# Kernel tuning notes

Measured on AMD Instinct MI355X. Metric: run time of the kernel, lower is better.

Reference implementation:

```python
import jax, jax.numpy as jnp
import numpy as np
from jax import lax

EPS = 1e-5
SLOPE = 0.1
BETA = 0.25


def lrelu(x):
    return jnp.where(x >= 0, x, SLOPE * x)


def bn(x, g, b):
    # training-mode BatchNorm2d: batch stats over (N, H, W), biased variance
    m = x.mean((0, 2, 3), keepdims=True)
    v = x.var((0, 2, 3), keepdims=True)
    return g[None, :, None, None] * (x - m) * lax.rsqrt(v + EPS) + b[None, :, None, None]


def conv2d(x, w, b, stride=1, pad=1):
    y = lax.conv_general_dilated(x, w, (stride, stride), [(pad, pad), (pad, pad)],
                                 dimension_numbers=('NCHW', 'OIHW', 'NCHW'))
    return y + b[None, :, None, None]


def conv_transpose2d(x, w, b):
    # torch ConvTranspose2d(k=3, stride=2, padding=1, output_padding=1): out = 2*in
    # implemented as conv of stride-dilated input with spatially-flipped, IO-swapped kernel
    wt = jnp.flip(w, (2, 3)).transpose(1, 0, 2, 3)  # (in,out,kh,kw) -> (out,in,kh,kw)
    y = lax.conv_general_dilated(x, wt, (1, 1), [(1, 2), (1, 2)], lhs_dilation=(2, 2),
                                 dimension_numbers=('NCHW', 'OIHW', 'NCHW'))
    return y + b[None, :, None, None]


def vqvae_forward(x, cb, e1_w, e1_b, bn1_g, bn1_b, e2_w, e2_b, bn2_g, bn2_b,
                  preq_w, preq_b, postq_w, postq_b,
                  d1_w, d1_b, bn3_g, bn3_b, d2_w, d2_b, bn4_g, bn4_b, d3_w, d3_b):
    # encoder
    h = lrelu(bn(conv2d(x, e1_w, e1_b, stride=2), bn1_g, bn1_b))
    h = lrelu(bn(conv2d(h, e2_w, e2_b, stride=2), bn2_g, bn2_b))
    pq = conv2d(h, preq_w, preq_b)  # (B, cb_dim, H, W)
    B, C, H, W = pq.shape
    z = pq.transpose(0, 2, 3, 1).reshape(-1, C)  # (B*H*W, C)
    # squared euclidean distances (argmin equals cdist argmin)
    d2 = ((z * z).sum(-1, keepdims=True) - 2.0 * z @ cb.T + (cb * cb).sum(-1)[None, :])
    idx = jnp.argmin(d2, axis=-1)  # (B*H*W,)
    q = cb[idx]  # gather, (B*H*W, C)
    codebook_loss = jnp.mean((lax.stop_gradient(z) - q) ** 2)
    commitment_loss = jnp.mean((lax.stop_gradient(q) - z) ** 2)
    quantized_loss = codebook_loss + BETA * commitment_loss
    q_st = z + lax.stop_gradient(q - z)  # straight-through
    zq = q_st.reshape(B, H, W, C).transpose(0, 3, 1, 2)
    # decoder
    h = conv2d(zq, postq_w, postq_b)
    h = lrelu(bn(conv_transpose2d(h, d1_w, d1_b), bn3_g, bn3_b))
    h = lrelu(bn(conv_transpose2d(h, d2_w, d2_b), bn4_g, bn4_b))
    out = jnp.tanh(conv2d(h, d3_w, d3_b))
    return out, quantized_loss


def setup_inputs() -> dict:
    key = jax.random.key(0)
    ks = jax.random.split(key, 16)
    f32 = jnp.float32
    K, D, CC = 1024, 64, 3

    def w(k, shape, fan_in):
        return (jax.random.normal(k, shape, f32) / np.sqrt(fan_in)).astype(f32)

    inp = {
        'x': jax.random.normal(ks[0], (16, CC, 256, 256), f32),
        'cb': jax.random.normal(ks[1], (K, D), f32),
        'e1_w': w(ks[2], (16, CC, 3, 3), CC * 9), 'e1_b': jnp.zeros((16,), f32),
        'bn1_g': jnp.ones((16,), f32), 'bn1_b': jnp.zeros((16,), f32),
        'e2_w': w(ks[3], (4, 16, 3, 3), 16 * 9), 'e2_b': jnp.zeros((4,), f32),
        'bn2_g': jnp.ones((4,), f32), 'bn2_b': jnp.zeros((4,), f32),
        'preq_w': w(ks[4], (D, 4, 3, 3), 4 * 9), 'preq_b': jnp.zeros((D,), f32),
        'postq_w': w(ks[5], (4, D, 3, 3), D * 9), 'postq_b': jnp.zeros((4,), f32),
        'd1_w': w(ks[6], (4, 16, 3, 3), 4 * 9), 'd1_b': jnp.zeros((16,), f32),  # (in,out,kh,kw)
        'bn3_g': jnp.ones((16,), f32), 'bn3_b': jnp.zeros((16,), f32),
        'd2_w': w(ks[7], (16, 32, 3, 3), 16 * 9), 'd2_b': jnp.zeros((32,), f32),
        'bn4_g': jnp.ones((32,), f32), 'bn4_b': jnp.zeros((32,), f32),
        'd3_w': w(ks[8], (CC, 32, 3, 3), 32 * 9), 'd3_b': jnp.zeros((CC,), f32),
    }
    return inp


def reference(x, cb, e1_w, e1_b, bn1_g, bn1_b, e2_w, e2_b, bn2_g, bn2_b,
              preq_w, preq_b, postq_w, postq_b,
              d1_w, d1_b, bn3_g, bn3_b, d2_w, d2_b, bn4_g, bn4_b, d3_w, d3_b):
    return vqvae_forward(x, cb, e1_w, e1_b, bn1_g, bn1_b, e2_w, e2_b, bn2_g, bn2_b,
                         preq_w, preq_b, postq_w, postq_b,
                         d1_w, d1_b, bn3_g, bn3_b, d2_w, d2_b, bn4_g, bn4_b, d3_w, d3_b)
```

## Files before the change

kernel.cpp:

```cpp
#include <hip/hip_runtime.h>
#include <math.h>

#define EPSV 1e-5
#define SLOPE 0.1f

typedef __attribute__((ext_vector_type(4))) float f32x4;
typedef __attribute__((ext_vector_type(8))) short short8x;

__device__ __forceinline__ float lrelu(float x){ return x >= 0.f ? x : SLOPE * x; }
__device__ __forceinline__ float tanh_fast(float x){
  float e = __expf(2.f * x);
  return 1.f - 2.f / (e + 1.f);
}
__device__ __forceinline__ unsigned bf16rne(float f){
  unsigned u = __float_as_uint(f);
  u += 0x7fff + ((u >> 16) & 1);
  return u >> 16;
}

template<int CL>
__device__ __forceinline__ void stats_epilogue(const float* sums, const float* sqs,
    double* __restrict__ part, int chbase, int P, int p, float* sred){
  const int C2 = 2 * CL;
  int t = threadIdx.x;
  #pragma unroll
  for (int c = 0; c < CL; c++){
    sred[t * C2 + c] = sums[c];
    sred[t * C2 + CL + c] = sqs[c];
  }
  __syncthreads();
  if (t < 64){
    int c = t % C2;
    int g = t / C2;
    const int G = 64 / C2;
    const int R = 256 / G;
    double s = 0;
    for (int r = g * R; r < (g + 1) * R; r++) s += (double)sred[r * C2 + c];
    #pragma unroll
    for (int off = C2; off < 64; off <<= 1) s += __shfl_xor(s, off);
    if (t < C2){
      int ch = chbase + (c < CL ? c : c - CL);
      part[(size_t)ch * 2 * P + (c < CL ? 0 : P) + p] = s;
    }
  }
}

__global__ __launch_bounds__(256) void bn_red_fin(const double* __restrict__ part, int P,
    const float* __restrict__ g, const float* __restrict__ b, float* __restrict__ ss, int C, double count){
  int c = blockIdx.x;
  __shared__ double r0[256], r1[256];
  int t = threadIdx.x;
  double s = 0, q = 0;
  for (int p = t; p < P; p += 256){
    s += part[(size_t)c * 2 * P + p];
    q += part[(size_t)c * 2 * P + P + p];
  }
  r0[t] = s; r1[t] = q; __syncthreads();
  for (int o = 128; o > 0; o >>= 1){
    if (t < o){ r0[t] += r0[t + o]; r1[t] += r1[t + o]; }
    __syncthreads();
  }
  if (t == 0){
    double m = r0[0] / count;
    double var = r1[0] / count - m * m;
    double scale = (double)g[c] / sqrt(var + EPSV);
    ss[c] = (float)scale;
    ss[C + c] = (float)((double)b[c] - m * scale);
  }
}

__global__ __launch_bounds__(256) void e1_conv(const float* __restrict__ x, const float* __restrict__ w,
    const float* __restrict__ bias, float* __restrict__ out, double* __restrict__ part){
  int idx = blockIdx.x * 256 + threadIdx.x;
  int ox2 = idx & 63, oy = (idx >> 6) & 127, n = idx >> 13;
  float acc[16][2];
  #pragma unroll
  for (int co = 0; co < 16; co++){ float b = bias[co]; acc[co][0] = b; acc[co][1] = b; }
  int ix0 = 4 * ox2 - 1;
  int lclamp = (ox2 > 0) ? ix0 : 0;
  const float* xp = x + (size_t)n * 3 * 65536;
  #pragma unroll
  for (int ci = 0; ci < 3; ci++){
    const float* pl = xp + ci * 65536;
    #pragma unroll
    for (int ky = 0; ky < 3; ky++){
      int iy = 2 * oy - 1 + ky;
      if (iy >= 0){
        const float* row = pl + iy * 256;
        float l = row[lclamp];
        float4 m = *(const float4*)(row + ix0 + 1);
        float v0 = (ox2 > 0) ? l : 0.f;
        #pragma unroll
        for (int co = 0; co < 16; co++){
          const float* wp = w + ((co * 3 + ci) * 3 + ky) * 3;
          acc[co][0] = fmaf(v0,  wp[0], acc[co][0]);
          acc[co][0] = fmaf(m.x, wp[1], acc[co][0]);
          acc[co][0] = fmaf(m.y, wp[2], acc[co][0]);
          acc[co][1] = fmaf(m.y, wp[0], acc[co][1]);
          acc[co][1] = fmaf(m.z, wp[1], acc[co][1]);
          acc[co][1] = fmaf(m.w, wp[2], acc[co][1]);
        }
      }
    }
  }
  float sums[16], sqs[16];
  #pragma unroll
  for (int co = 0; co < 16; co++){
    float2 st; st.x = acc[co][0]; st.y = acc[co][1];
    *(float2*)(out + ((size_t)(n * 16 + co) * 128 + oy) * 128 + 2 * ox2) = st;
    sums[co] = acc[co][0] + acc[co][1];
    sqs[co] = acc[co][0] * acc[co][0] + acc[co][1] * acc[co][1];
  }
  __shared__ float sred[256 * 32];
  stats_epilogue<16>(sums, sqs, part, 0, 512, blockIdx.x, sred);
}

__global__ __launch_bounds__(256) void e2_conv(const float* __restrict__ in, const float* __restrict__ w,
    const float* __restrict__ bias, const float* __restrict__ ssIn, float* __restrict__ out,
    double* __restrict__ part){
  int idx = blockIdx.x * 256 + threadIdx.x;
  int ox = idx & 63, oy = (idx >> 6) & 63, n = idx >> 12;
  float acc[4];
  #pragma unroll
  for (int j = 0; j < 4; j++) acc[j] = bias[j];
  int iy0 = oy * 2 - 1, ix0 = ox * 2 - 1;
  const float* ip = in + (size_t)n * 16 * 16384;
  #pragma unroll
  for (int ky = 0; ky < 3; ky++){
    int iy = iy0 + ky; if ((unsigned)iy >= 128u) continue;
    #pragma unroll
    for (int kx = 0; kx < 3; kx++){
      int ix = ix0 + kx; if ((unsigned)ix >= 128u) continue;
      const float* r = ip + iy * 128 + ix;
      #pragma unroll
      for (int ci = 0; ci < 16; ci++){
        float v = lrelu(fmaf(r[ci * 16384], ssIn[ci], ssIn[16 + ci]));
        #pragma unroll
        for (int co = 0; co < 4; co++)
          acc[co] = fmaf(v, w[(co * 16 + ci) * 9 + ky * 3 + kx], acc[co]);
      }
    }
  }
  float sums[4], sqs[4];
  #pragma unroll
  for (int co = 0; co < 4; co++){
    out[(((size_t)n * 4 + co) * 64 + oy) * 64 + ox] = acc[co];
    sums[co] = acc[co];
    sqs[co] = acc[co] * acc[co];
  }
  __shared__ float sred[256 * 8];
  stats_epilogue<4>(sums, sqs, part, 0, 256, blockIdx.x, sred);
}

__global__ __launch_bounds__(256) void preq_conv(const float* __restrict__ in, const float* __restrict__ w,
    const float* __restrict__ bias, const float* __restrict__ ssIn, float* __restrict__ Zq){
  int idx = blockIdx.x * 256 + threadIdx.x;
  int sp = idx & 65535;
  int coq = idx >> 16;
  int x = sp & 63, y = (sp >> 6) & 63, n = sp >> 12;
  float scv[4] = {ssIn[0], ssIn[1], ssIn[2], ssIn[3]};
  float shv[4] = {ssIn[4], ssIn[5], ssIn[6], ssIn[7]};
  float a0 = bias[coq * 4 + 0], a1 = bias[coq * 4 + 1], a2 = bias[coq * 4 + 2], a3 = bias[coq * 4 + 3];
  const float* ip = in + (size_t)n * 4 * 4096;
  #pragma unroll
  for (int ky = 0; ky < 3; ky++){
    int iy = y - 1 + ky; if ((unsigned)iy >= 64u) continue;
    #pragma unroll
    for (int kx = 0; kx < 3; kx++){
      int ix = x - 1 + kx; if ((unsigned)ix >= 64u) continue;
      #pragma unroll
      for (int ci = 0; ci < 4; ci++){
        float v = lrelu(fmaf(ip[ci * 4096 + iy * 64 + ix], scv[ci], shv[ci]));
        const float* wp = w + ((coq * 4) * 4 + ci) * 9 + ky * 3 + kx;
        a0 = fmaf(v, wp[0], a0);
        a1 = fmaf(v, wp[36], a1);
        a2 = fmaf(v, wp[72], a2);
        a3 = fmaf(v, wp[108], a3);
      }
    }
  }
  float4 o; o.x = a0; o.y = a1; o.z = a2; o.w = a3;
  ((float4*)Zq)[coq * 65536 + sp] = o;
}

__global__ __launch_bounds__(256) void prep_all(const float* __restrict__ cb, double* __restrict__ cb64,
    double* __restrict__ cbn64, float* __restrict__ cbn32, unsigned short* __restrict__ cbh,
    unsigned short* __restrict__ cbl, int* __restrict__ flagcnt,
    const float* __restrict__ pw, float* __restrict__ P){
  int t = threadIdx.x;
  if (blockIdx.x < 4){
    int k = blockIdx.x * 256 + t;
    if (k == 0) flagcnt[0] = 0;
    double s = 0;
    for (int d = 0; d < 64; d++){
      float v = cb[k * 64 + d];
      cb64[(size_t)k * 64 + d] = (double)v;
      s = fma((double)v, (double)v, s);
      unsigned h = bf16rne(v);
      float hf = __uint_as_float(h << 16);
      unsigned l = bf16rne(v - hf);
      cbh[k * 64 + d] = (unsigned short)h;
      cbl[k * 64 + d] = (unsigned short)l;
    }
    cbn64[k] = s;
    cbn32[k] = (float)s;
  } else {
    int gid = (blockIdx.x - 4) * 256 + t;
    if (gid >= 9216) return;
    int k = gid / 9, tap = gid - k * 9;
    float a0 = 0.f, a1 = 0.f, a2 = 0.f, a3 = 0.f;
    const float* cp = cb + (k << 6);
    #pragma unroll 16
    for (int ci = 0; ci < 64; ci++){
      float c = cp[ci];
      a0 = fmaf(c, pw[(0 * 64 + ci) * 9 + tap], a0);
      a1 = fmaf(c, pw[(1 * 64 + ci) * 9 + tap], a1);
      a2 = fmaf(c, pw[(2 * 64 + ci) * 9 + tap], a2);
      a3 = fmaf(c, pw[(3 * 64 + ci) * 9 + tap], a3);
    }
    float4 o; o.x = a0; o.y = a1; o.z = a2; o.w = a3;
    ((float4*)P)[gid] = o;
  }
}

__global__ __launch_bounds__(256) void vq_screen_mfma(const float* __restrict__ Zq,
    const unsigned short* __restrict__ cbh, const unsigned short* __restrict__ cbl,
    const float* __restrict__ cbn32, int* __restrict__ idxout,
    int* __restrict__ flagcnt, int* __restrict__ flaglist){
  __shared__ unsigned short lcb[32 * 64 * 8];
  __shared__ float lcn[128];
  int t = threadIdx.x;
  int lane = t & 63;
  int w = t >> 6;
  int col = lane & 15, hg = lane >> 4;
  int pos0 = blockIdx.x * 128 + w * 32;
  int posA = pos0 + col, posB = pos0 + 16 + col;
  const float4* Zq4 = (const float4*)Zq;
  short8x zhA[2], zlA[2], zhB[2], zlB[2];
  #pragma unroll
  for (int kc = 0; kc < 2; kc++){
    #pragma unroll
    for (int s = 0; s < 2; s++){
      int pos = s ? posB : posA;
      float4 f0 = Zq4[(size_t)(8 * kc + 2 * hg) * 65536 + pos];
      float4 f1 = Zq4[(size_t)(8 * kc + 2 * hg + 1) * 65536 + pos];
      float zv[8] = {f0.x, f0.y, f0.z, f0.w, f1.x, f1.y, f1.z, f1.w};
      union { unsigned u[4]; short8x v; } H, L;
      #pragma unroll
      for (int j = 0; j < 4; j++){
        unsigned h0 = bf16rne(zv[2 * j]);
        unsigned h1 = bf16rne(zv[2 * j + 1]);
        float hf0 = __uint_as_float(h0 << 16);
        float hf1 = __uint_as_float(h1 << 16);
        unsigned l0 = bf16rne(zv[2 * j] - hf0);
        unsigned l1 = bf16rne(zv[2 * j + 1] - hf1);
        H.u[j] = h0 | (h1 << 16);
        L.u[j] = l0 | (l1 << 16);
      }
      if (s){ zhB[kc] = H.v; zlB[kc] = L.v; } else { zhA[kc] = H.v; zlA[kc] = L.v; }
    }
  }
  float bestA = 3.0e38f, secA = 3.0e38f, bestB = 3.0e38f, secB = 3.0e38f;
  int biA = 0, biB = 0;
  for (int step = 0; step < 8; step++){
    int code0 = step * 128;
    __syncthreads();
    #pragma unroll
    for (int i = 0; i < 8; i++){
      int piece = i * 256 + t;
      int fb = piece >> 6, pl = piece & 63;
      int g = fb >> 2, kc = (fb >> 1) & 1, sp = fb & 1;
      const unsigned short* src = (sp ? cbl : cbh)
          + ((size_t)(code0 + g * 16 + (pl & 15)) << 6) + kc * 32 + ((pl >> 4) << 3);
      *(uint4*)&lcb[piece * 8] = *(const uint4*)src;
    }
    if (t < 128) lcn[t] = cbn32[code0 + t];
    __syncthreads();
    #pragma unroll 2
    for (int g = 0; g < 8; g++){
      const short8x* lc8 = (const short8x*)lcb;
      short8x Ah0 = lc8[(g * 4 + 0) * 64 + lane];
      short8x Al0 = lc8[(g * 4 + 1) * 64 + lane];
      short8x Ah1 = lc8[(g * 4 + 2) * 64 + lane];
      short8x Al1 = lc8[(g * 4 + 3) * 64 + lane];
      f32x4 accA = {0.f, 0.f, 0.f, 0.f};
      f32x4 accB = {0.f, 0.f, 0.f, 0.f};
      accA = __builtin_amdgcn_mfma_f32_16x16x32_bf16(Ah0, zhA[0], accA, 0, 0, 0);
      accA = __builtin_amdgcn_mfma_f32_16x16x32_bf16(Ah1, zhA[1], accA, 0, 0, 0);
      accA = __builtin_amdgcn_mfma_f32_16x16x32_bf16(Ah0, zlA[0], accA, 0, 0, 0);
      accA = __builtin_amdgcn_mfma_f32_16x16x32_bf16(Ah1, zlA[1], accA, 0, 0, 0);
      accA = __builtin_amdgcn_mfma_f32_16x16x32_bf16(Al0, zhA[0], accA, 0, 0, 0);
      accA = __builtin_amdgcn_mfma_f32_16x16x32_bf16(Al1, zhA[1], accA, 0, 0, 0);
      accB = __builtin_amdgcn_mfma_f32_16x16x32_bf16(Ah0, zhB[0], accB, 0, 0, 0);
      accB = __builtin_amdgcn_mfma_f32_16x16x32_bf16(Ah1, zhB[1], accB, 0, 0, 0);
      accB = __builtin_amdgcn_mfma_f32_16x16x32_bf16(Ah0, zlB[0], accB, 0, 0, 0);
      accB = __builtin_amdgcn_mfma_f32_16x16x32_bf16(Ah1, zlB[1], accB, 0, 0, 0);
      accB = __builtin_amdgcn_mfma_f32_16x16x32_bf16(Al0, zhB[0], accB, 0, 0, 0);
      accB = __builtin_amdgcn_mfma_f32_16x16x32_bf16(Al1, zhB[1], accB, 0, 0, 0);
      int cbase = code0 + g * 16 + 4 * hg;
      #pragma unroll
      for (int r = 0; r < 4; r++){
        float cn = lcn[g * 16 + 4 * hg + r];
        float sA = fmaf(accA[r], -2.0f, cn);
        float mA = fmaxf(sA, bestA);
        secA = fminf(secA, mA);
        if (sA < bestA){ bestA = sA; biA = cbase + r; }
        float sB = fmaf(accB[r], -2.0f, cn);
        float mB = fmaxf(sB, bestB);
        secB = fminf(secB, mB);
        if (sB < bestB){ bestB = sB; biB = cbase + r; }
      }
    }
  }
  #pragma unroll
  for (int off = 16; off <= 32; off <<= 1){
    float ob = __shfl_xor(bestA, off);
    float os = __shfl_xor(secA, off);
    int oi = __shfl_xor(biA, off);
    secA = fminf(fminf(secA, os), fmaxf(bestA, ob));
    if (ob < bestA){ bestA = ob; biA = oi; }
    ob = __shfl_xor(bestB, off);
    os = __shfl_xor(secB, off);
    oi = __shfl_xor(biB, off);
    secB = fminf(fminf(secB, os), fmaxf(bestB, ob));
    if (ob < bestB){ bestB = ob; biB = oi; }
  }
  if (hg == 0){
    idxout[posA] = biA;
    if (secA - bestA < 1.2e-2f){
      int slot = atomicAdd(flagcnt, 1);
      flaglist[slot] = posA;
    }
    idxout[posB] = biB;
    if (secB - bestB < 1.2e-2f){
      int slot = atomicAdd(flagcnt, 1);
      flaglist[slot] = posB;
    }
  }
}

__global__ __launch_bounds__(256) void vq_refine(const float* __restrict__ Zq, const double* __restrict__ cb64,
    const double* __restrict__ cbn64, const int* __restrict__ flagcnt, const int* __restrict__ flaglist,
    int* __restrict__ idxout){
  int gw = (blockIdx.x * 256 + threadIdx.x) >> 6;
  int lane = threadIdx.x & 63;
  int nf = flagcnt[0];
  for (int f = gw; f < nf; f += 512){
    int pos = flaglist[f];
    float zr[64];
    #pragma unroll
    for (int q = 0; q < 16; q++){
      float4 v = ((const float4*)Zq)[q * 65536 + pos];
      zr[4 * q] = v.x; zr[4 * q + 1] = v.y; zr[4 * q + 2] = v.z; zr[4 * q + 3] = v.w;
    }
    double best = 1e300; int bi = 1 << 30;
    for (int k = lane; k < 1024; k += 64){
      const double* c = cb64 + (size_t)k * 64;
      double a0 = 0, a1 = 0, a2 = 0, a3 = 0;
      #pragma unroll
      for (int d = 0; d < 64; d += 4){
        a0 = fma(c[d], (double)zr[d], a0);
        a1 = fma(c[d + 1], (double)zr[d + 1], a1);
        a2 = fma(c[d + 2], (double)zr[d + 2], a2);
        a3 = fma(c[d + 3], (double)zr[d + 3], a3);
      }
      double s = cbn64[k] - 2.0 * ((a0 + a1) + (a2 + a3));
      if (s < best){ best = s; bi = k; }
    }
    #pragma unroll
    for (int o = 32; o > 0; o >>= 1){
      double ob = __shfl_xor(best, o);
      int oi = __shfl_xor(bi, o);
      if (ob < best || (ob == best && oi < bi)){ best = ob; bi = oi; }
    }
    if (lane == 0) idxout[pos] = bi;
  }
}

__global__ __launch_bounds__(256) void postq_gather(const float* __restrict__ P, const int* __restrict__ idxm,
    const float* __restrict__ bias, float* __restrict__ out,
    const float* __restrict__ Zq, const float* __restrict__ cb, double* __restrict__ losspart){
  int gid = blockIdx.x * 256 + threadIdx.x;
  int sp = gid & 65535;
  int co = gid >> 16;
  co = __builtin_amdgcn_readfirstlane(co);
  int xx = sp & 63, yy = (sp >> 6) & 63, n = sp >> 12;
  float acc = bias[co];
  #pragma unroll
  for (int ky = 0; ky < 3; ky++){
    int iy = yy - 1 + ky; if ((unsigned)iy >= 64u) continue;
    #pragma unroll
    for (int kx = 0; kx < 3; kx++){
      int ix = xx - 1 + kx; if ((unsigned)ix >= 64u) continue;
      int spt = (n << 12) + (iy << 6) + ix;
      int k = idxm[spt];
      acc += P[(k * 9 + (ky * 3 + kx)) * 4 + co];
    }
  }
  out[((size_t)(n * 4 + co) << 12) + (yy << 6) + xx] = acc;
  if (co == 0){
    int k = idxm[sp];
    const float4* c4 = (const float4*)(cb + (k << 6));
    double l = 0;
    #pragma unroll
    for (int q = 0; q < 16; q++){
      float4 z = ((const float4*)Zq)[q * 65536 + sp];
      float4 c = c4[q];
      float d0 = z.x - c.x, d1 = z.y - c.y, d2 = z.z - c.z, d3 = z.w - c.w;
      l += (double)d0 * d0 + (double)d1 * d1 + (double)d2 * d2 + (double)d3 * d3;
    }
    __shared__ double sb[256];
    int t = threadIdx.x;
    sb[t] = l; __syncthreads();
    for (int o = 128; o > 0; o >>= 1){
      if (t < o) sb[t] += sb[t + o];
      __syncthreads();
    }
    if (t == 0) losspart[blockIdx.x] = sb[0];
  }
}

template<int CI, int CO, int IHt, int IWt, bool APPLY>
__global__ __launch_bounds__(256) void convT_cob8(const float* __restrict__ in, const float* __restrict__ w,
    const float* __restrict__ bias, const float* __restrict__ ssIn, float* __restrict__ out,
    double* __restrict__ part){
  constexpr int SB = IHt * IWt / 256;
  constexpr int COG = CO / 8;
  constexpr int P = 16 * SB;
  const int OW = IWt * 2;
  int idx = blockIdx.x * 256 + threadIdx.x;
  int ix = idx % IWt, iy = (idx / IWt) % IHt;
  int cog = (idx / (IWt * IHt)) % COG, n = idx / (IWt * IHt * COG);
  cog = __builtin_amdgcn_readfirstlane(cog);
  n   = __builtin_amdgcn_readfirstlane(n);
  float a00[8], a01[8], a10[8], a11[8];
  #pragma unroll
  for (int j = 0; j < 8; j++){ float b = bias[cog * 8 + j]; a00[j] = b; a01[j] = b; a10[j] = b; a11[j] = b; }
  bool okx = (ix + 1 < IWt), oky = (iy + 1 < IHt);
  int ixp = okx ? ix + 1 : ix, iyp = oky ? iy + 1 : iy;
  const float* ip = in + (size_t)n * CI * IHt * IWt;
  #pragma unroll 4
  for (int ci = 0; ci < CI; ci++){
    const float* p = ip + ci * IHt * IWt;
    float v00 = p[iy * IWt + ix];
    float v01 = p[iy * IWt + ixp];
    float v10 = p[iyp * IWt + ix];
    float v11 = p[iyp * IWt + ixp];
    if (APPLY){
      float sc = ssIn[ci], sh = ssIn[CI + ci];
      v00 = lrelu(fmaf(v00, sc, sh));
      v01 = lrelu(fmaf(v01, sc, sh));
      v10 = lrelu(fmaf(v10, sc, sh));
      v11 = lrelu(fmaf(v11, sc, sh));
    }
    if (!okx) v01 = 0.f;
    if (!oky) v10 = 0.f;
    if (!(okx && oky)) v11 = 0.f;
    const float* wp = w + ((size_t)ci * CO + cog * 8) * 9;
    #pragma unroll
    for (int j = 0; j < 8; j++){
      const float* q = wp + j * 9;
      a00[j] = fmaf(q[4], v00, a00[j]);
      a01[j] = fmaf(q[3], v01, a01[j]); a01[j] = fmaf(q[5], v00, a01[j]);
      a10[j] = fmaf(q[1], v10, a10[j]); a10[j] = fmaf(q[7], v00, a10[j]);
      a11[j] = fmaf(q[0], v11, a11[j]); a11[j] = fmaf(q[2], v10, a11[j]);
      a11[j] = fmaf(q[6], v01, a11[j]); a11[j] = fmaf(q[8], v00, a11[j]);
    }
  }
  float sums[8], sqs[8];
  #pragma unroll
  for (int j = 0; j < 8; j++){
    float* o = out + (((size_t)n * CO + cog * 8 + j) * (IHt * 2) + 2 * iy) * OW + 2 * ix;
    float2 r0; r0.x = a00[j]; r0.y = a01[j];
    float2 r1; r1.x = a10[j]; r1.y = a11[j];
    *(float2*)o = r0;
    *(float2*)(o + OW) = r1;
    sums[j] = (a00[j] + a01[j]) + (a10[j] + a11[j]);
    sqs[j] = (a00[j] * a00[j] + a01[j] * a01[j]) + (a10[j] * a10[j] + a11[j] * a11[j]);
  }
  __shared__ float sred[256 * 16];
  int sb = blockIdx.x % SB;
  stats_epilogue<8>(sums, sqs, part, cog * 8, P, n * SB + sb, sred);
}

__global__ __launch_bounds__(256) void d3_tile(const float* __restrict__ F, const float* __restrict__ w,
    const float* __restrict__ bias, const float* __restrict__ ss, float* __restrict__ out,
    const double* __restrict__ losspart){
  __shared__ float st[4 * 6 * 256];
  int t = threadIdx.x;
  int xg = t & 63, r = t >> 6;
  int n = blockIdx.x >> 6, oyb = blockIdx.x & 63;
  int oy = oyb * 4 + r;
  if (blockIdx.x == 0 && t < 64){
    double s = losspart[t] + losspart[t + 64] + losspart[t + 128] + losspart[t + 192];
    #pragma unroll
    for (int o = 32; o > 0; o >>= 1) s += __shfl_xor(s, o);
    if (t == 0) out[3145728] = (float)(1.25 * s / (65536.0 * 64.0));
  }
  float acc[3][4];
  #pragma unroll
  for (int co = 0; co < 3; co++){
    float b = bias[co];
    #pragma unroll
    for (int j = 0; j < 4; j++) acc[co][j] = b;
  }
  const float* base = F + (size_t)n * 32 * 65536;
  for (int cc = 0; cc < 8; cc++){
    int cib = cc * 4;
    #pragma unroll
    for (int j = 0; j < 6; j++){
      int p = j * 256 + t;
      int cl = p / 384, rem = p - cl * 384;
      int rr = rem >> 6, xq = rem & 63;
      int g = oyb * 4 - 1 + rr;
      float4 v;
      if ((unsigned)g < 256u){
        v = *(const float4*)(base + ((size_t)(cib + cl) * 256 + g) * 256 + 4 * xq);
        float sc = ss[cib + cl], sh = ss[32 + cib + cl];
        v.x = lrelu(fmaf(v.x, sc, sh));
        v.y = lrelu(fmaf(v.y, sc, sh));
        v.z = lrelu(fmaf(v.z, sc, sh));
        v.w = lrelu(fmaf(v.w, sc, sh));
      } else {
        v.x = 0.f; v.y = 0.f; v.z = 0.f; v.w = 0.f;
      }
      *(float4*)&st[((cl * 6 + rr) << 8) | (4 * xq)] = v;
    }
    __syncthreads();
    #pragma unroll
    for (int cl = 0; cl < 4; cl++){
      #pragma unroll
      for (int ky = 0; ky < 3; ky++){
        int rr = r + ky;
        float4 A = *(const float4*)&st[((cl * 6 + rr) << 8) | (4 * xg)];
        float Lv = __shfl_up(A.w, 1);
        float Rv = __shfl_down(A.x, 1);
        float u0 = (xg == 0) ? 0.f : Lv;
        float u5 = (xg == 63) ? 0.f : Rv;
        float u[6] = {u0, A.x, A.y, A.z, A.w, u5};
        #pragma unroll
        for (int co = 0; co < 3; co++){
          const float* wp = w + ((co * 32 + cib + cl) * 9) + ky * 3;
          #pragma unroll
          for (int j = 0; j < 4; j++){
            acc[co][j] = fmaf(u[j],     wp[0], acc[co][j]);
            acc[co][j] = fmaf(u[j + 1], wp[1], acc[co][j]);
            acc[co][j] = fmaf(u[j + 2], wp[2], acc[co][j]);
          }
        }
      }
    }
    __syncthreads();
  }
  #pragma unroll
  for (int co = 0; co < 3; co++){
    float4 s0;
    s0.x = tanh_fast(acc[co][0]); s0.y = tanh_fast(acc[co][1]);
    s0.z = tanh_fast(acc[co][2]); s0.w = tanh_fast(acc[co][3]);
    float* o = out + ((size_t)(n * 3 + co) * 256 + oy) * 256 + 4 * xg;
    *(float4*)o = s0;
  }
}

extern "C" void kernel_launch(void* const* d_in, const int* in_sizes, int n_in,
                              void* d_out, int out_size, void* d_ws, size_t ws_size,
                              hipStream_t stream){
  const float* x      = (const float*)d_in[0];
  const float* cb     = (const float*)d_in[1];
  const float* e1_w   = (const float*)d_in[2];
  const float* e1_b   = (const float*)d_in[3];
  const float* bn1_g  = (const float*)d_in[4];
  const float* bn1_b  = (const float*)d_in[5];
  const float* e2_w   = (const float*)d_in[6];
  const float* e2_b   = (const float*)d_in[7];
  const float* bn2_g  = (const float*)d_in[8];
  const float* bn2_b  = (const float*)d_in[9];
  const float* preq_w = (const float*)d_in[10];
  const float* preq_b = (const float*)d_in[11];
  const float* postq_w= (const float*)d_in[12];
  const float* postq_b= (const float*)d_in[13];
  const float* d1_w   = (const float*)d_in[14];
  const float* d1_b   = (const float*)d_in[15];
  const float* bn3_g  = (const float*)d_in[16];
  const float* bn3_b  = (const float*)d_in[17];
  const float* d2_w   = (const float*)d_in[18];
  const float* d2_b   = (const float*)d_in[19];
  const float* bn4_g  = (const float*)d_in[20];
  const float* bn4_b  = (const float*)d_in[21];
  const float* d3_w   = (const float*)d_in[22];
  const float* d3_b   = (const float*)d_in[23];
  float* out = (float*)d_out;
  char* ws = (char*)d_ws;

  double* losspart = (double*)ws;
  int*    flagcnt  = (int*)(ws + 2048);
  float*  ss       = (float*)(ws + 4096);
  double* cb64     = (double*)(ws + 8192);
  double* cbn64    = (double*)(ws + 532480);
  float*  cbn32    = (float*)(ws + 540672);
  unsigned short* cbh = (unsigned short*)(ws + 544768);
  unsigned short* cbl = (unsigned short*)(ws + 675840);
  int*    flaglist = (int*)(ws + 806912);
  int*    idx      = (int*)(ws + 1069056);
  double* part_e1  = (double*)(ws + 1331200);
  double* part_e2  = (double*)(ws + 1462272);
  float*  Ptab     = (float*)(ws + 1478656);
  double* part_d1  = (double*)(ws + 1478656);
  double* part_d2  = (double*)(ws + 1544192);
  float*  A        = (float*)(ws + 2097152);
  float*  B        = (float*)(ws + 18874368);
  float*  Zq       = (float*)(ws + 19922944);
  float*  F        = (float*)(ws + 36700160);

  float *ss1 = ss + 0, *ss2 = ss + 32, *ss3 = ss + 48, *ss4 = ss + 80;
  float* D = B;

  prep_all<<<40, 256, 0, stream>>>(cb, cb64, cbn64, cbn32, cbh, cbl, flagcnt, postq_w, Ptab);

  e1_conv<<<512, 256, 0, stream>>>(x, e1_w, e1_b, A, part_e1);
  bn_red_fin<<<16, 256, 0, stream>>>(part_e1, 512, bn1_g, bn1_b, ss1, 16, 262144.0);
  e2_conv<<<256, 256, 0, stream>>>(A, e2_w, e2_b, ss1, B, part_e2);
  bn_red_fin<<<4, 256, 0, stream>>>(part_e2, 256, bn2_g, bn2_b, ss2, 4, 65536.0);
  preq_conv<<<4096, 256, 0, stream>>>(B, preq_w, preq_b, ss2, Zq);

  vq_screen_mfma<<<512, 256, 0, stream>>>(Zq, cbh, cbl, cbn32, idx, flagcnt, flaglist);
  vq_refine<<<128, 256, 0, stream>>>(Zq, cb64, cbn64, flagcnt, flaglist, idx);

  postq_gather<<<1024, 256, 0, stream>>>(Ptab, idx, postq_b, D, Zq, cb, losspart);
  convT_cob8<4, 16, 64, 64, false><<<512, 256, 0, stream>>>(D, d1_w, d1_b, nullptr, A, part_d1);
  bn_red_fin<<<16, 256, 0, stream>>>(part_d1, 256, bn3_g, bn3_b, ss3, 16, 262144.0);
  convT_cob8<16, 32, 128, 128, true><<<4096, 256, 0, stream>>>(A, d2_w, d2_b, ss3, F, part_d2);
  bn_red_fin<<<32, 256, 0, stream>>>(part_d2, 1024, bn4_g, bn4_b, ss4, 32, 1048576.0);
  d3_tile<<<1024, 256, 0, stream>>>(F, d3_w, d3_b, ss4, out, losspart);
}
```

Measured before the change: 308.0 us.

## Prune VQ refine to candidate code chunks and widen convT to two input columns

The screen kernel now writes each position's per-128-code-chunk best distance to a workspace buffer. The refine kernel reads these values and runs fp64 distances only for chunks whose best lies within the ambiguity margin, instead of scanning all 1024 codes. Separately, the transposed-conv kernel now has each thread handle two adjacent input columns, sharing loads and emitting float4 stores, with half the blocks. This adds register pressure and extra workspace traffic, and relies on the chunk-level bound being a safe pruning test.

```diff
diff --git a/kernel.cpp b/kernel.cpp
--- a/kernel.cpp
+++ b/kernel.cpp
@@ -226,7 +226,7 @@
 __global__ __launch_bounds__(256) void vq_screen_mfma(const float* __restrict__ Zq,
     const unsigned short* __restrict__ cbh, const unsigned short* __restrict__ cbl,
     const float* __restrict__ cbn32, int* __restrict__ idxout,
-    int* __restrict__ flagcnt, int* __restrict__ flaglist){
+    int* __restrict__ flagcnt, int* __restrict__ flaglist, float* __restrict__ stepb){
   __shared__ unsigned short lcb[32 * 64 * 8];
   __shared__ float lcn[128];
   int t = threadIdx.x;
@@ -240,8 +240,8 @@
   #pragma unroll
   for (int kc = 0; kc < 2; kc++){
     #pragma unroll
-    for (int s = 0; s < 2; s++){
-      int pos = s ? posB : posA;
+    for (int tb = 0; tb < 2; tb++){
+      int pos = tb ? posB : posA;
       float4 f0 = Zq4[(size_t)(8 * kc + 2 * hg) * 65536 + pos];
       float4 f1 = Zq4[(size_t)(8 * kc + 2 * hg + 1) * 65536 + pos];
       float zv[8] = {f0.x, f0.y, f0.z, f0.w, f1.x, f1.y, f1.z, f1.w};
@@ -257,11 +257,11 @@
         H.u[j] = h0 | (h1 << 16);
         L.u[j] = l0 | (l1 << 16);
       }
-      if (s){ zhB[kc] = H.v; zlB[kc] = L.v; } else { zhA[kc] = H.v; zlA[kc] = L.v; }
-    }
-  }
-  float bestA = 3.0e38f, secA = 3.0e38f, bestB = 3.0e38f, secB = 3.0e38f;
-  int biA = 0, biB = 0;
+      if (tb){ zhB[kc] = H.v; zlB[kc] = L.v; } else { zhA[kc] = H.v; zlA[kc] = L.v; }
+    }
+  }
+  float BA = 3.0e38f, SA = 3.0e38f, BB = 3.0e38f, SBt = 3.0e38f;
+  int IA = 0, IB = 0;
   for (int step = 0; step < 8; step++){
     int code0 = step * 128;
     __syncthreads();
@@ -276,6 +276,8 @@
     }
     if (t < 128) lcn[t] = cbn32[code0 + t];
     __syncthreads();
+    float bA = 3.0e38f, sA = 3.0e38f, bB = 3.0e38f, sB = 3.0e38f;
+    int iA = 0, iB = 0;
     #pragma unroll 2
     for (int g = 0; g < 8; g++){
       const short8x* lc8 = (const short8x*)lcb;
@@ -301,38 +303,42 @@
       #pragma unroll
       for (int r = 0; r < 4; r++){
         float cn = lcn[g * 16 + 4 * hg + r];
-        float sA = fmaf(accA[r], -2.0f, cn);
-        float mA = fmaxf(sA, bestA);
-        secA = fminf(secA, mA);
-        if (sA < bestA){ bestA = sA; biA = cbase + r; }
-        float sB = fmaf(accB[r], -2.0f, cn);
-        float mB = fmaxf(sB, bestB);
-        secB = fminf(secB, mB);
-        if (sB < bestB){ bestB = sB; biB = cbase + r; }
-      }
-    }
-  }
-  #pragma unroll
-  for (int off = 16; off <= 32; off <<= 1){
-    float ob = __shfl_xor(bestA, off);
-    float os = __shfl_xor(secA, off);
-    int oi = __shfl_xor(biA, off);
-    secA = fminf(fminf(secA, os), fmaxf(bestA, ob));
-    if (ob < bestA){ bestA = ob; biA = oi; }
-    ob = __shfl_xor(bestB, off);
-    os = __shfl_xor(secB, off);
-    oi = __shfl_xor(biB, off);
-    secB = fminf(fminf(secB, os), fmaxf(bestB, ob));
-    if (ob < bestB){ bestB = ob; biB = oi; }
+        float vA = fmaf(accA[r], -2.0f, cn);
+        sA = fminf(sA, fmaxf(vA, bA));
+        if (vA < bA){ bA = vA; iA = cbase + r; }
+        float vB = fmaf(accB[r], -2.0f, cn);
+        sB = fminf(sB, fmaxf(vB, bB));
+        if (vB < bB){ bB = vB; iB = cbase + r; }
+      }
+    }
+    #pragma unroll
+    for (int off = 16; off <= 32; off <<= 1){
+      float ob = __shfl_xor(bA, off);
+      float os = __shfl_xor(sA, off);
+      int oi = __shfl_xor(iA, off);
+      sA = fminf(fminf(sA, os), fmaxf(bA, ob));
+      if (ob < bA){ bA = ob; iA = oi; }
+      ob = __shfl_xor(bB, off);
+      os = __shfl_xor(sB, off);
+      oi = __shfl_xor(iB, off);
+      sB = fminf(fminf(sB, os), fmaxf(bB, ob));
+      if (ob < bB){ bB = ob; iB = oi; }
+    }
+    if (hg == 0){
+      stepb[step * 65536 + posA] = bA;
+      stepb[step * 65536 + posB] = bB;
+    }
+    if (bA < BA){ SA = fminf(BA, sA); BA = bA; IA = iA; } else SA = fminf(SA, bA);
+    if (bB < BB){ SBt = fminf(BB, sB); BB = bB; IB = iB; } else SBt = fminf(SBt, bB);
   }
   if (hg == 0){
-    idxout[posA] = biA;
-    if (secA - bestA < 1.2e-2f){
+    idxout[posA] = IA;
+    if (SA - BA < 1.2e-2f){
       int slot = atomicAdd(flagcnt, 1);
       flaglist[slot] = posA;
     }
-    idxout[posB] = biB;
-    if (secB - bestB < 1.2e-2f){
+    idxout[posB] = IB;
+    if (SBt - BB < 1.2e-2f){
       int slot = atomicAdd(flagcnt, 1);
       flaglist[slot] = posB;
     }
@@ -341,7 +347,7 @@
 
 __global__ __launch_bounds__(256) void vq_refine(const float* __restrict__ Zq, const double* __restrict__ cb64,
     const double* __restrict__ cbn64, const int* __restrict__ flagcnt, const int* __restrict__ flaglist,
-    int* __restrict__ idxout){
+    const float* __restrict__ stepb, int* __restrict__ idxout){
   int gw = (blockIdx.x * 256 + threadIdx.x) >> 6;
   int lane = threadIdx.x & 63;
   int nf = flagcnt[0];
@@ -353,19 +359,32 @@
       float4 v = ((const float4*)Zq)[q * 65536 + pos];
       zr[4 * q] = v.x; zr[4 * q + 1] = v.y; zr[4 * q + 2] = v.z; zr[4 * q + 3] = v.w;
     }
+    float sb[8];
+    float B = 3.0e38f;
+    #pragma unroll
+    for (int s = 0; s < 8; s++){ sb[s] = stepb[s * 65536 + pos]; B = fminf(B, sb[s]); }
+    float lim = B + 1.2e-2f;
     double best = 1e300; int bi = 1 << 30;
-    for (int k = lane; k < 1024; k += 64){
-      const double* c = cb64 + (size_t)k * 64;
-      double a0 = 0, a1 = 0, a2 = 0, a3 = 0;
-      #pragma unroll
-      for (int d = 0; d < 64; d += 4){
-        a0 = fma(c[d], (double)zr[d], a0);
-        a1 = fma(c[d + 1], (double)zr[d + 1], a1);
-        a2 = fma(c[d + 2], (double)zr[d + 2], a2);
-        a3 = fma(c[d + 3], (double)zr[d + 3], a3);
-      }
-      double s = cbn64[k] - 2.0 * ((a0 + a1) + (a2 + a3));
-      if (s < best){ best = s; bi = k; }
+    #pragma unroll
+    for (int s = 0; s < 8; s++){
+      if (sb[s] < lim){
+        int k0 = s * 128 + 2 * lane;
+        #pragma unroll
+        for (int kk = 0; kk < 2; kk++){
+          int k = k0 + kk;
+          const double* c = cb64 + (size_t)k * 64;
+          double a0 = 0, a1 = 0, a2 = 0, a3 = 0;
+          #pragma unroll
+          for (int d = 0; d < 64; d += 4){
+            a0 = fma(c[d], (double)zr[d], a0);
+            a1 = fma(c[d + 1], (double)zr[d + 1], a1);
+            a2 = fma(c[d + 2], (double)zr[d + 2], a2);
+            a3 = fma(c[d + 3], (double)zr[d + 3], a3);
+          }
+          double sc = cbn64[k] - 2.0 * ((a0 + a1) + (a2 + a3));
+          if (sc < best){ best = sc; bi = k; }
+        }
+      }
     }
     #pragma unroll
     for (int o = 32; o > 0; o >>= 1){
@@ -421,66 +440,82 @@
 }
 
 template<int CI, int CO, int IHt, int IWt, bool APPLY>
-__global__ __launch_bounds__(256) void convT_cob8(const float* __restrict__ in, const float* __restrict__ w,
+__global__ __launch_bounds__(256) void convT_w2(const float* __restrict__ in, const float* __restrict__ w,
     const float* __restrict__ bias, const float* __restrict__ ssIn, float* __restrict__ out,
     double* __restrict__ part){
-  constexpr int SB = IHt * IWt / 256;
+  constexpr int IWH = IWt / 2;
   constexpr int COG = CO / 8;
+  constexpr int SB = IHt * IWH * COG / 256;
   constexpr int P = 16 * SB;
   const int OW = IWt * 2;
   int idx = blockIdx.x * 256 + threadIdx.x;
-  int ix = idx % IWt, iy = (idx / IWt) % IHt;
-  int cog = (idx / (IWt * IHt)) % COG, n = idx / (IWt * IHt * COG);
+  int ixp = idx % IWH;
+  int iy = (idx / IWH) % IHt;
+  int cog = (idx / (IWH * IHt)) % COG;
+  int n = idx / (IWH * IHt * COG);
   cog = __builtin_amdgcn_readfirstlane(cog);
   n   = __builtin_amdgcn_readfirstlane(n);
-  float a00[8], a01[8], a10[8], a11[8];
-  #pragma unroll
-  for (int j = 0; j < 8; j++){ float b = bias[cog * 8 + j]; a00[j] = b; a01[j] = b; a10[j] = b; a11[j] = b; }
-  bool okx = (ix + 1 < IWt), oky = (iy + 1 < IHt);
-  int ixp = okx ? ix + 1 : ix, iyp = oky ? iy + 1 : iy;
+  float a[8][8];
+  #pragma unroll
+  for (int j = 0; j < 8; j++){
+    float b = bias[cog * 8 + j];
+    #pragma unroll
+    for (int q = 0; q < 8; q++) a[j][q] = b;
+  }
+  bool oky = (iy + 1 < IHt);
+  bool okx = (2 * ixp + 2 < IWt);
+  int iyp = oky ? iy + 1 : iy;
+  int xe = okx ? 2 : 0;
   const float* ip = in + (size_t)n * CI * IHt * IWt;
   #pragma unroll 4
   for (int ci = 0; ci < CI; ci++){
-    const float* p = ip + ci * IHt * IWt;
-    float v00 = p[iy * IWt + ix];
-    float v01 = p[iy * IWt + ixp];
-    float v10 = p[iyp * IWt + ix];
-    float v11 = p[iyp * IWt + ixp];
+    const float* r0 = ip + ci * IHt * IWt + iy * IWt + 2 * ixp;
+    const float* r1 = ip + ci * IHt * IWt + iyp * IWt + 2 * ixp;
+    float2 va = *(const float2*)r0;
+    float ve = r0[xe];
+    float2 vb = *(const float2*)r1;
+    float vf = r1[xe];
     if (APPLY){
       float sc = ssIn[ci], sh = ssIn[CI + ci];
-      v00 = lrelu(fmaf(v00, sc, sh));
-      v01 = lrelu(fmaf(v01, sc, sh));
-      v10 = lrelu(fmaf(v10, sc, sh));
-      v11 = lrelu(fmaf(v11, sc, sh));
-    }
-    if (!okx) v01 = 0.f;
-    if (!oky) v10 = 0.f;
-    if (!(okx && oky)) v11 = 0.f;
+      va.x = lrelu(fmaf(va.x, sc, sh));
+      va.y = lrelu(fmaf(va.y, sc, sh));
+      ve   = lrelu(fmaf(ve,   sc, sh));
+      vb.x = lrelu(fmaf(vb.x, sc, sh));
+      vb.y = lrelu(fmaf(vb.y, sc, sh));
+      vf   = lrelu(fmaf(vf,   sc, sh));
+    }
+    if (!okx){ ve = 0.f; vf = 0.f; }
+    if (!oky){ vb.x = 0.f; vb.y = 0.f; vf = 0.f; }
     const float* wp = w + ((size_t)ci * CO + cog * 8) * 9;
     #pragma unroll
     for (int j = 0; j < 8; j++){
       const float* q = wp + j * 9;
-      a00[j] = fmaf(q[4], v00, a00[j]);
-      a01[j] = fmaf(q[3], v01, a01[j]); a01[j] = fmaf(q[5], v00, a01[j]);
-      a10[j] = fmaf(q[1], v10, a10[j]); a10[j] = fmaf(q[7], v00, a10[j]);
-      a11[j] = fmaf(q[0], v11, a11[j]); a11[j] = fmaf(q[2], v10, a11[j]);
-      a11[j] = fmaf(q[6], v01, a11[j]); a11[j] = fmaf(q[8], v00, a11[j]);
+      a[j][0] = fmaf(q[4], va.x, a[j][0]);
+      a[j][1] = fmaf(q[3], va.y, a[j][1]); a[j][1] = fmaf(q[5], va.x, a[j][1]);
+      a[j][2] = fmaf(q[1], vb.x, a[j][2]); a[j][2] = fmaf(q[7], va.x, a[j][2]);
+      a[j][3] = fmaf(q[0], vb.y, a[j][3]); a[j][3] = fmaf(q[2], vb.x, a[j][3]);
+      a[j][3] = fmaf(q[6], va.y, a[j][3]); a[j][3] = fmaf(q[8], va.x, a[j][3]);
+      a[j][4] = fmaf(q[4], va.y, a[j][4]);
+      a[j][5] = fmaf(q[3], ve,   a[j][5]); a[j][5] = fmaf(q[5], va.y, a[j][5]);
+      a[j][6] = fmaf(q[1], vb.y, a[j][6]); a[j][6] = fmaf(q[7], va.y, a[j][6]);
+      a[j][7] = fmaf(q[0], vf,   a[j][7]); a[j][7] = fmaf(q[2], vb.y, a[j][7]);
+      a[j][7] = fmaf(q[6], ve,   a[j][7]); a[j][7] = fmaf(q[8], va.y, a[j][7]);
     }
   }
   float sums[8], sqs[8];
   #pragma unroll
   for (int j = 0; j < 8; j++){
-    float* o = out + (((size_t)n * CO + cog * 8 + j) * (IHt * 2) + 2 * iy) * OW + 2 * ix;
-    float2 r0; r0.x = a00[j]; r0.y = a01[j];
-    float2 r1; r1.x = a10[j]; r1.y = a11[j];
-    *(float2*)o = r0;
-    *(float2*)(o + OW) = r1;
-    sums[j] = (a00[j] + a01[j]) + (a10[j] + a11[j]);
-    sqs[j] = (a00[j] * a00[j] + a01[j] * a01[j]) + (a10[j] * a10[j] + a11[j] * a11[j]);
+    float4 R0; R0.x = a[j][0]; R0.y = a[j][1]; R0.z = a[j][4]; R0.w = a[j][5];
+    float4 R1; R1.x = a[j][2]; R1.y = a[j][3]; R1.z = a[j][6]; R1.w = a[j][7];
+    float* o = out + (((size_t)n * CO + cog * 8 + j) * (IHt * 2) + 2 * iy) * OW + 4 * ixp;
+    *(float4*)o = R0;
+    *(float4*)(o + OW) = R1;
+    sums[j] = ((a[j][0] + a[j][1]) + (a[j][2] + a[j][3])) + ((a[j][4] + a[j][5]) + (a[j][6] + a[j][7]));
+    sqs[j]  = ((a[j][0]*a[j][0] + a[j][1]*a[j][1]) + (a[j][2]*a[j][2] + a[j][3]*a[j][3]))
+            + ((a[j][4]*a[j][4] + a[j][5]*a[j][5]) + (a[j][6]*a[j][6] + a[j][7]*a[j][7]));
   }
   __shared__ float sred[256 * 16];
-  int sb = blockIdx.x % SB;
-  stats_epilogue<8>(sums, sqs, part, cog * 8, P, n * SB + sb, sred);
+  stats_epilogue<8>(sums, sqs, part, cog * 8, P, n * SB + (blockIdx.x % SB), sred);
 }
 
 __global__ __launch_bounds__(256) void d3_tile(const float* __restrict__ F, const float* __restrict__ w,
@@ -606,11 +641,12 @@
   double* part_e2  = (double*)(ws + 1462272);
   float*  Ptab     = (float*)(ws + 1478656);
   double* part_d1  = (double*)(ws + 1478656);
-  double* part_d2  = (double*)(ws + 1544192);
   float*  A        = (float*)(ws + 2097152);
   float*  B        = (float*)(ws + 18874368);
   float*  Zq       = (float*)(ws + 19922944);
+  double* part_d2  = (double*)(ws + 19922944);
   float*  F        = (float*)(ws + 36700160);
+  float*  stepb    = (float*)(ws + 36700160);
 
   float *ss1 = ss + 0, *ss2 = ss + 32, *ss3 = ss + 48, *ss4 = ss + 80;
   float* D = B;
@@ -623,13 +659,13 @@
   bn_red_fin<<<4, 256, 0, stream>>>(part_e2, 256, bn2_g, bn2_b, ss2, 4, 65536.0);
   preq_conv<<<4096, 256, 0, stream>>>(B, preq_w, preq_b, ss2, Zq);
 
-  vq_screen_mfma<<<512, 256, 0, stream>>>(Zq, cbh, cbl, cbn32, idx, flagcnt, flaglist);
-  vq_refine<<<128, 256, 0, stream>>>(Zq, cb64, cbn64, flagcnt, flaglist, idx);
+  vq_screen_mfma<<<512, 256, 0, stream>>>(Zq, cbh, cbl, cbn32, idx, flagcnt, flaglist, stepb);
+  vq_refine<<<128, 256, 0, stream>>>(Zq, cb64, cbn64, flagcnt, flaglist, stepb, idx);
 
   postq_gather<<<1024, 256, 0, stream>>>(Ptab, idx, postq_b, D, Zq, cb, losspart);
-  convT_cob8<4, 16, 64, 64, false><<<512, 256, 0, stream>>>(D, d1_w, d1_b, nullptr, A, part_d1);
+  convT_w2<4, 16, 64, 64, false><<<256, 256, 0, stream>>>(D, d1_w, d1_b, nullptr, A, part_d1);
   bn_red_fin<<<16, 256, 0, stream>>>(part_d1, 256, bn3_g, bn3_b, ss3, 16, 262144.0);
-  convT_cob8<16, 32, 128, 128, true><<<4096, 256, 0, stream>>>(A, d2_w, d2_b, ss3, F, part_d2);
-  bn_red_fin<<<32, 256, 0, stream>>>(part_d2, 1024, bn4_g, bn4_b, ss4, 32, 1048576.0);
+  convT_w2<16, 32, 128, 128, true><<<2048, 256, 0, stream>>>(A, d2_w, d2_b, ss3, F, part_d2);
+  bn_red_fin<<<32, 256, 0, stream>>>(part_d2, 2048, bn4_g, bn4_b, ss4, 32, 1048576.0);
   d3_tile<<<1024, 256, 0, stream>>>(F, d3_w, d3_b, ss4, out, losspart);
 }
```

New measurement: 301.7 us. 2.0% less time.
